# Performance work log

Measured on AMD Instinct MI355X. Metric: run time of the kernel, lower is better.

## Reference

```python
import jax, jax.numpy as jnp
import numpy as np

HIDDEN = 1024
HEADS = 16
HEAD_D = HIDDEN // HEADS
FILL = -10000.0


def setup_inputs() -> dict:
    key = jax.random.key(0)
    ks = jax.random.split(key, 5)
    scale = 1.0 / np.sqrt(HIDDEN)
    x = jax.random.normal(ks[0], (2, 2048, HIDDEN), dtype=jnp.float32)
    # nn.Linear weights stored as [in, out] (already transposed vs torch)
    W_qkv = jax.random.uniform(ks[1], (HIDDEN, 3 * HIDDEN), dtype=jnp.float32, minval=-scale, maxval=scale)
    b_qkv = jax.random.uniform(ks[2], (3 * HIDDEN,), dtype=jnp.float32, minval=-scale, maxval=scale)
    W_o = jax.random.uniform(ks[3], (HIDDEN, HIDDEN), dtype=jnp.float32, minval=-scale, maxval=scale)
    b_o = jax.random.uniform(ks[4], (HIDDEN,), dtype=jnp.float32, minval=-scale, maxval=scale)
    return {"x": x, "W_qkv": W_qkv, "b_qkv": b_qkv, "W_o": W_o, "b_o": b_o}


def reference(x, W_qkv, b_qkv, W_o, b_o):
    b, s, _ = x.shape
    qkv = x @ W_qkv + b_qkv                       # [b, s, 3*hidden]
    q, k, v = jnp.split(qkv, 3, axis=-1)
    # [b, s, hidden] -> [b, h, s, d]
    def to_heads(t):
        return t.reshape(b, s, HEADS, HEAD_D).transpose(0, 2, 1, 3)
    q, k, v = to_heads(q), to_heads(k), to_heads(v)
    logits = jnp.einsum('bhqd,bhkd->bhqk', q, k) / np.sqrt(HEAD_D).astype(np.float32)
    # Faithful to the original: tril, then fill anything equal to 0 (incl.
    # genuine zeros) with the masked_logit_fill value.
    logits_tril = jnp.tril(logits)
    logits_masked = jnp.where(logits_tril == 0.0, jnp.float32(FILL), logits_tril)
    probs = jax.nn.softmax(logits_masked, axis=-1)
    pre_o = jnp.einsum('bhqk,bhkd->bhqd', probs, v)    # [b, h, s, d]
    pre_o = pre_o.transpose(0, 2, 1, 3).reshape(b, s, HIDDEN)
    return pre_o @ W_o + b_o
```

## Files before the change

kernel.cpp:

```cpp
#include <hip/hip_runtime.h>

typedef __attribute__((ext_vector_type(8))) short short8;
typedef __attribute__((ext_vector_type(4))) short short4b;
typedef __attribute__((ext_vector_type(4))) float f32x4;

static __device__ __forceinline__ short f2bf(float f) {
    unsigned u = __builtin_bit_cast(unsigned, f);
    u += 0x7FFFu + ((u >> 16) & 1u);
    return (short)(u >> 16);
}

static __device__ __forceinline__ void g2l16(const void* g, void* l) {
    __builtin_amdgcn_global_load_lds(
        (const __attribute__((address_space(1))) unsigned*)g,
        (__attribute__((address_space(3))) unsigned*)l, 16, 0, 0);
}

__global__ void convert_x(const float* __restrict__ x, short* __restrict__ xb, int n4) {
    int i = blockIdx.x * blockDim.x + threadIdx.x;
    if (i >= n4) return;
    f32x4 v = *(const f32x4*)&x[(long)i * 4];
    short4b o;
    #pragma unroll
    for (int j = 0; j < 4; ++j) o[j] = f2bf(v[j]);
    *(short4b*)&xb[(long)i * 4] = o;
}

__global__ void transpose_conv(const float* __restrict__ W, short* __restrict__ Wt,
                               int K, int N) {
    __shared__ float lds[64][65];
    const int t = threadIdx.x;
    const int n0 = blockIdx.x * 64, k0 = blockIdx.y * 64;
    const int rr = t >> 4, q4 = (t & 15) * 4;
    #pragma unroll
    for (int p = 0; p < 4; ++p) {
        int k = rr + p * 16;
        f32x4 v = *(const f32x4*)&W[(long)(k0 + k) * N + n0 + q4];
        #pragma unroll
        for (int j = 0; j < 4; ++j) lds[k][q4 + j] = v[j];
    }
    __syncthreads();
    #pragma unroll
    for (int p = 0; p < 4; ++p) {
        int nloc = rr + p * 16;
        short4b o;
        #pragma unroll
        for (int j = 0; j < 4; ++j) o[j] = f2bf(lds[q4 + j][nloc]);
        *(short4b*)&Wt[(long)(n0 + nloc) * K + k0 + q4] = o;
    }
}

template<int F32OUT, int QSCALE>
__global__ __launch_bounds__(256, 2)
void gemm_bt(const short* __restrict__ A, const short* __restrict__ Bt,
             const float* __restrict__ bias, void* __restrict__ C,
             int M, int N, int K) {
    __shared__ short lA[128 * 32];
    __shared__ short lB[128 * 32];
    const int t = threadIdx.x;
    const int lane = t & 63, w = t >> 6;
    const int m0 = blockIdx.y * 128, n0 = blockIdx.x * 128;
    const int lr = lane & 15, lk = lane >> 4;
    const int wr = w >> 1, wc = w & 1;

    f32x4 acc[4][4];
    #pragma unroll
    for (int i = 0; i < 4; ++i)
        #pragma unroll
        for (int j = 0; j < 4; ++j)
            #pragma unroll
            for (int e = 0; e < 4; ++e) acc[i][j][e] = 0.0f;

    const int nsteps = K >> 5;
    for (int kt = 0; kt < nsteps; ++kt) {
        const int kb = kt * 32;
        #pragma unroll
        for (int c = 0; c < 2; ++c) {
            int off  = c * 4096 + w * 1024;
            int offl = off + lane * 16;
            int ra = offl >> 6;
            int ca = (offl & 63) >> 1;
            g2l16(A  + (long)(m0 + ra) * K + kb + ca, (short*)lA + (off >> 1));
            g2l16(Bt + (long)(n0 + ra) * K + kb + ca, (short*)lB + (off >> 1));
        }
        __syncthreads();
        short8 af[4], bf[4];
        #pragma unroll
        for (int m = 0; m < 4; ++m)
            af[m] = *(const short8*)&lA[(wr * 64 + m * 16 + lr) * 32 + lk * 8];
        #pragma unroll
        for (int n = 0; n < 4; ++n)
            bf[n] = *(const short8*)&lB[(wc * 64 + n * 16 + lr) * 32 + lk * 8];
        #pragma unroll
        for (int m = 0; m < 4; ++m)
            #pragma unroll
            for (int n = 0; n < 4; ++n)
                acc[m][n] = __builtin_amdgcn_mfma_f32_16x16x32_bf16(af[m], bf[n], acc[m][n], 0, 0, 0);
        __syncthreads();
    }

    #pragma unroll
    for (int n = 0; n < 4; ++n) {
        int col = n0 + wc * 64 + n * 16 + lr;
        float bb = bias[col];
        float sc = (QSCALE && col < 1024) ? 0.125f : 1.0f;
        #pragma unroll
        for (int m = 0; m < 4; ++m) {
            int rowb = m0 + wr * 64 + m * 16 + lk * 4;
            #pragma unroll
            for (int r = 0; r < 4; ++r) {
                float v = (acc[m][n][r] + bb) * sc;
                if (F32OUT) ((float*)C)[(long)(rowb + r) * N + col] = v;
                else        ((short*)C)[(long)(rowb + r) * N + col] = f2bf(v);
            }
        }
    }
}

__global__ void build_vt(const short* __restrict__ qkv, short* __restrict__ vt) {
    __shared__ short lds[64][72];
    const int t = threadIdx.x;
    const int st = blockIdx.x, bh = blockIdx.y;
    const int b = bh >> 4, h = bh & 15;
    const int s0 = st * 64;
    const int sr = t >> 3, c8 = (t & 7) * 8;
    #pragma unroll
    for (int p = 0; p < 2; ++p) {
        int s = sr + p * 32;
        short8 v = *(const short8*)&qkv[(long)(b * 2048 + s0 + s) * 3072 + 2048 + h * 64 + c8];
        *(short8*)&lds[s][c8] = v;
    }
    __syncthreads();
    #pragma unroll
    for (int p = 0; p < 2; ++p) {
        int d = sr + p * 32;
        short8 v;
        #pragma unroll
        for (int j = 0; j < 8; ++j) v[j] = lds[c8 + j][d];
        *(short8*)&vt[(long)(bh * 64 + d) * 2048 + s0 + c8] = v;
    }
}

__global__ __launch_bounds__(256, 4)
void attn_kernel(const short* __restrict__ qkv, const short* __restrict__ vt,
                 short* __restrict__ pre_o) {
    __shared__ short lK[2][64 * 64];
    __shared__ short lV[2][64 * 64];
    __shared__ short lP[4][16 * 64];
    const int t = threadIdx.x, lane = t & 63, w = t >> 6;
    const int lr = lane & 15, lk = lane >> 4;
    const int Q = 31 - blockIdx.x;
    const int bh = blockIdx.y;
    const int b = bh >> 4, h = bh & 15;
    const int q0 = Q * 64;
    const int nt = Q + 1;

    int soff[2], sRow[2], sCol[2];
    #pragma unroll
    for (int c = 0; c < 2; ++c) {
        int off  = c * 4096 + w * 1024;
        int offl = off + lane * 16;
        int r    = offl >> 7;
        soff[c]  = off >> 1;
        sRow[c]  = r;
        sCol[c]  = (((offl >> 4) & 7) ^ (r & 7)) * 8;
    }

    short8 aq[2];
    #pragma unroll
    for (int dk = 0; dk < 2; ++dk)
        aq[dk] = *(const short8*)&qkv[(long)(b * 2048 + q0 + w * 16 + lr) * 3072
                                      + h * 64 + dk * 32 + lk * 8];

    f32x4 accO[4];
    #pragma unroll
    for (int n = 0; n < 4; ++n)
        #pragma unroll
        for (int e = 0; e < 4; ++e) accO[n][e] = 0.0f;
    float mst[4], lst[4];
    #pragma unroll
    for (int r = 0; r < 4; ++r) { mst[r] = -1e30f; lst[r] = 0.0f; }

    #pragma unroll
    for (int c = 0; c < 2; ++c) {
        g2l16(qkv + (long)(b * 2048 + sRow[c]) * 3072 + 1024 + h * 64 + sCol[c],
              &lK[0][soff[c]]);
        g2l16(vt + (long)(bh * 64 + sRow[c]) * 2048 + sCol[c],
              &lV[0][soff[c]]);
    }
    __syncthreads();

    #pragma unroll 1
    for (int kt = 0; kt < nt; ++kt) {
        const int cur = kt & 1;
        if (kt + 1 < nt) {
            #pragma unroll
            for (int c = 0; c < 2; ++c) {
                g2l16(qkv + (long)(b * 2048 + (kt + 1) * 64 + sRow[c]) * 3072
                          + 1024 + h * 64 + sCol[c],
                      &lK[cur ^ 1][soff[c]]);
                g2l16(vt + (long)(bh * 64 + sRow[c]) * 2048 + (kt + 1) * 64 + sCol[c],
                      &lV[cur ^ 1][soff[c]]);
            }
        }

        f32x4 accS[4];
        #pragma unroll
        for (int n = 0; n < 4; ++n) {
            #pragma unroll
            for (int e = 0; e < 4; ++e) accS[n][e] = 0.0f;
            #pragma unroll
            for (int dk = 0; dk < 2; ++dk) {
                short8 bk = *(const short8*)((const char*)&lK[cur][0]
                             + (n * 16 + lr) * 128 + (((dk * 4 + lk) ^ (lr & 7)) << 4));
                accS[n] = __builtin_amdgcn_mfma_f32_16x16x32_bf16(aq[dk], bk, accS[n], 0, 0, 0);
            }
        }

        const bool diag = (kt == nt - 1);
        #pragma unroll
        for (int r = 0; r < 4; ++r) {
            int qrow = q0 + w * 16 + lk * 4 + r;
            float sv[4];
            #pragma unroll
            for (int n = 0; n < 4; ++n) {
                float s = accS[n][r];
                if (diag) {
                    int key = kt * 64 + n * 16 + lr;
                    if (key > qrow || s == 0.0f) s = -10000.0f;
                } else {
                    if (s == 0.0f) s = -10000.0f;
                }
                sv[n] = s;
            }
            float mx = fmaxf(fmaxf(sv[0], sv[1]), fmaxf(sv[2], sv[3]));
            mx = fmaxf(mx, __shfl_xor(mx, 1));
            mx = fmaxf(mx, __shfl_xor(mx, 2));
            mx = fmaxf(mx, __shfl_xor(mx, 4));
            mx = fmaxf(mx, __shfl_xor(mx, 8));
            float mnew = fmaxf(mst[r], mx);
            float corr = __expf(mst[r] - mnew);
            mst[r] = mnew;
            float rs = 0.0f;
            #pragma unroll
            for (int n = 0; n < 4; ++n) { float p = __expf(sv[n] - mnew); sv[n] = p; rs += p; }
            rs += __shfl_xor(rs, 1);
            rs += __shfl_xor(rs, 2);
            rs += __shfl_xor(rs, 4);
            rs += __shfl_xor(rs, 8);
            lst[r] = lst[r] * corr + rs;
            #pragma unroll
            for (int n = 0; n < 4; ++n) accO[n][r] *= corr;
            int prr = lk * 4 + r;
            int swz = (prr & 7) << 4;
            #pragma unroll
            for (int n = 0; n < 4; ++n) {
                int pc = n * 16 + lr;
                *(short*)((char*)&lP[w][0] + prr * 128 + ((pc * 2) ^ swz)) = f2bf(sv[n]);
            }
        }

        short8 ap[2];
        #pragma unroll
        for (int kk = 0; kk < 2; ++kk)
            ap[kk] = *(const short8*)((const char*)&lP[w][0] + lr * 128
                                      + (((kk * 4 + lk) ^ (lr & 7)) << 4));
        #pragma unroll
        for (int n = 0; n < 4; ++n)
            #pragma unroll
            for (int kk = 0; kk < 2; ++kk) {
                short8 bv = *(const short8*)((const char*)&lV[cur][0]
                             + (n * 16 + lr) * 128 + (((kk * 4 + lk) ^ (lr & 7)) << 4));
                accO[n] = __builtin_amdgcn_mfma_f32_16x16x32_bf16(ap[kk], bv, accO[n], 0, 0, 0);
            }

        __syncthreads();
    }

    #pragma unroll
    for (int r = 0; r < 4; ++r) {
        int qrow = q0 + w * 16 + lk * 4 + r;
        float inv = 1.0f / lst[r];
        #pragma unroll
        for (int n = 0; n < 4; ++n)
            pre_o[(long)(b * 2048 + qrow) * 1024 + h * 64 + n * 16 + lr] =
                f2bf(accO[n][r] * inv);
    }
}

extern "C" void kernel_launch(void* const* d_in, const int* in_sizes, int n_in,
                              void* d_out, int out_size, void* d_ws, size_t ws_size,
                              hipStream_t stream) {
    const float* x    = (const float*)d_in[0];
    const float* Wqkv = (const float*)d_in[1];
    const float* bqkv = (const float*)d_in[2];
    const float* Wo   = (const float*)d_in[3];
    const float* bo   = (const float*)d_in[4];
    float* out = (float*)d_out;

    char* ws = (char*)d_ws;
    short* xb    = (short*)(ws);
    short* wqkvT = (short*)(ws + (8L  << 20));
    short* woT   = (short*)(ws + (14L << 20));
    short* qkv   = (short*)(ws + (16L << 20));
    short* vt    = (short*)(ws + (40L << 20));
    short* preo  = (short*)(ws + (48L << 20));

    convert_x<<<4096, 256, 0, stream>>>(x, xb, 4096 * 1024 / 4);
    transpose_conv<<<dim3(48, 16), 256, 0, stream>>>(Wqkv, wqkvT, 1024, 3072);
    transpose_conv<<<dim3(16, 16), 256, 0, stream>>>(Wo, woT, 1024, 1024);
    gemm_bt<0, 1><<<dim3(24, 32), 256, 0, stream>>>(xb, wqkvT, bqkv, qkv, 4096, 3072, 1024);
    build_vt<<<dim3(32, 32), 256, 0, stream>>>(qkv, vt);
    attn_kernel<<<dim3(32, 32), 256, 0, stream>>>(qkv, vt, preo);
    gemm_bt<1, 0><<<dim3(8, 32), 256, 0, stream>>>(preo, woT, bo, out, 4096, 1024, 1024);
}
```

Baseline: 260.8 us.

## Split long causal attention rows across two blocks and merge partial softmax results

The causal attention grid now has 44 column slots instead of 32. Query tiles 20–31, which have the longest key loops, are each split into two half-range blocks. Those blocks write unnormalized fp32 partial outputs plus running max and sum to workspace, and a new combine kernel merges them with log-sum-exp rescaling. The goal is to even out per-block work and cut the tail from the heaviest tiles, at the cost of an extra launch and fp32 partial traffic that reuses the xb workspace region.

```diff
diff --git a/kernel.cpp b/kernel.cpp
--- a/kernel.cpp
+++ b/kernel.cpp
@@ -143,17 +143,23 @@
 
 __global__ __launch_bounds__(256, 4)
 void attn_kernel(const short* __restrict__ qkv, const short* __restrict__ vt,
-                 short* __restrict__ pre_o) {
+                 short* __restrict__ pre_o, float* __restrict__ pO,
+                 float* __restrict__ pML) {
     __shared__ short lK[2][64 * 64];
     __shared__ short lV[2][64 * 64];
     __shared__ short lP[4][16 * 64];
     const int t = threadIdx.x, lane = t & 63, w = t >> 6;
     const int lr = lane & 15, lk = lane >> 4;
-    const int Q = 31 - blockIdx.x;
-    const int bh = blockIdx.y;
+    const int x = blockIdx.x, bh = blockIdx.y;
     const int b = bh >> 4, h = bh & 15;
+
+    int Q, kt0, kt1, half = -1;
+    if (x < 10)      { Q = 19 - x; kt0 = 0; kt1 = Q + 1; }
+    else if (x < 34) { int i = x - 10; Q = 31 - (i >> 1); half = i & 1;
+                       int h0 = (Q + 1) >> 1;
+                       kt0 = half ? h0 : 0; kt1 = half ? (Q + 1) : h0; }
+    else             { Q = 43 - x; kt0 = 0; kt1 = Q + 1; }
     const int q0 = Q * 64;
-    const int nt = Q + 1;
 
     int soff[2], sRow[2], sCol[2];
     #pragma unroll
@@ -183,17 +189,17 @@
 
     #pragma unroll
     for (int c = 0; c < 2; ++c) {
-        g2l16(qkv + (long)(b * 2048 + sRow[c]) * 3072 + 1024 + h * 64 + sCol[c],
+        g2l16(qkv + (long)(b * 2048 + kt0 * 64 + sRow[c]) * 3072 + 1024 + h * 64 + sCol[c],
               &lK[0][soff[c]]);
-        g2l16(vt + (long)(bh * 64 + sRow[c]) * 2048 + sCol[c],
+        g2l16(vt + (long)(bh * 64 + sRow[c]) * 2048 + kt0 * 64 + sCol[c],
               &lV[0][soff[c]]);
     }
     __syncthreads();
 
     #pragma unroll 1
-    for (int kt = 0; kt < nt; ++kt) {
-        const int cur = kt & 1;
-        if (kt + 1 < nt) {
+    for (int kt = kt0; kt < kt1; ++kt) {
+        const int cur = (kt - kt0) & 1;
+        if (kt + 1 < kt1) {
             #pragma unroll
             for (int c = 0; c < 2; ++c) {
                 g2l16(qkv + (long)(b * 2048 + (kt + 1) * 64 + sRow[c]) * 3072
@@ -217,7 +223,7 @@
             }
         }
 
-        const bool diag = (kt == nt - 1);
+        const bool diag = (kt == Q);
         #pragma unroll
         for (int r = 0; r < 4; ++r) {
             int qrow = q0 + w * 16 + lk * 4 + r;
@@ -277,14 +283,54 @@
         __syncthreads();
     }
 
-    #pragma unroll
-    for (int r = 0; r < 4; ++r) {
-        int qrow = q0 + w * 16 + lk * 4 + r;
-        float inv = 1.0f / lst[r];
-        #pragma unroll
-        for (int n = 0; n < 4; ++n)
-            pre_o[(long)(b * 2048 + qrow) * 1024 + h * 64 + n * 16 + lr] =
-                f2bf(accO[n][r] * inv);
+    if (half < 0) {
+        #pragma unroll
+        for (int r = 0; r < 4; ++r) {
+            int qrow = q0 + w * 16 + lk * 4 + r;
+            float inv = 1.0f / lst[r];
+            #pragma unroll
+            for (int n = 0; n < 4; ++n)
+                pre_o[(long)(b * 2048 + qrow) * 1024 + h * 64 + n * 16 + lr] =
+                    f2bf(accO[n][r] * inv);
+        }
+    } else {
+        const int g2 = ((Q - 20) * 32 + bh) * 2 + half;
+        float* U  = pO  + (long)g2 * 4096;
+        float* ML = pML + (long)g2 * 128;
+        #pragma unroll
+        for (int r = 0; r < 4; ++r) {
+            int row = w * 16 + lk * 4 + r;
+            #pragma unroll
+            for (int n = 0; n < 4; ++n)
+                U[row * 64 + n * 16 + lr] = accO[n][r];
+            if (lr == 0) { ML[row * 2] = mst[r]; ML[row * 2 + 1] = lst[r]; }
+        }
+    }
+}
+
+__global__ __launch_bounds__(256)
+void attn_combine(const float* __restrict__ pO, const float* __restrict__ pML,
+                  short* __restrict__ pre_o) {
+    const int g = blockIdx.x;
+    const int Q = 20 + (g >> 5), bh = g & 31, b = bh >> 4, h = bh & 15;
+    const int t = threadIdx.x;
+    const int row = t >> 2, d0 = (t & 3) * 16;
+    const float* ML0 = pML + ((long)(g * 2 + 0)) * 128 + row * 2;
+    const float* ML1 = pML + ((long)(g * 2 + 1)) * 128 + row * 2;
+    float m0 = ML0[0], l0 = ML0[1], m1 = ML1[0], l1 = ML1[1];
+    float m = fmaxf(m0, m1);
+    float e0 = __expf(m0 - m), e1 = __expf(m1 - m);
+    float inv = 1.0f / (l0 * e0 + l1 * e1);
+    const float* U0 = pO + ((long)(g * 2 + 0)) * 4096 + row * 64 + d0;
+    const float* U1 = pO + ((long)(g * 2 + 1)) * 4096 + row * 64 + d0;
+    long out = ((long)(b * 2048 + Q * 64 + row)) * 1024 + h * 64 + d0;
+    #pragma unroll
+    for (int j = 0; j < 16; j += 4) {
+        f32x4 a = *(const f32x4*)&U0[j];
+        f32x4 c = *(const f32x4*)&U1[j];
+        #pragma unroll
+        for (int e = 0; e < 4; ++e)
+            pre_o[out + j + e] = f2bf((a[e] * e0 + c[e] * e1) * inv);
     }
 }
 
@@ -305,12 +351,15 @@
     short* qkv   = (short*)(ws + (16L << 20));
     short* vt    = (short*)(ws + (40L << 20));
     short* preo  = (short*)(ws + (48L << 20));
+    float* pO    = (float*)(ws);
+    float* pML   = (float*)(ws + 12779520L);
 
     convert_x<<<4096, 256, 0, stream>>>(x, xb, 4096 * 1024 / 4);
     transpose_conv<<<dim3(48, 16), 256, 0, stream>>>(Wqkv, wqkvT, 1024, 3072);
     transpose_conv<<<dim3(16, 16), 256, 0, stream>>>(Wo, woT, 1024, 1024);
     gemm_bt<0, 1><<<dim3(24, 32), 256, 0, stream>>>(xb, wqkvT, bqkv, qkv, 4096, 3072, 1024);
     build_vt<<<dim3(32, 32), 256, 0, stream>>>(qkv, vt);
-    attn_kernel<<<dim3(32, 32), 256, 0, stream>>>(qkv, vt, preo);
+    attn_kernel<<<dim3(44, 32), 256, 0, stream>>>(qkv, vt, preo, pO, pML);
+    attn_combine<<<384, 256, 0, stream>>>(pO, pML, preo);
     gemm_bt<1, 0><<<dim3(8, 32), 256, 0, stream>>>(preo, woT, bo, out, 4096, 1024, 1024);
 }
```

Result: faster. 242.9 us (-6.9%).
